# Kernel tuning notes

Hardware: AMD Instinct MI355X
Metric: run time of the kernel (lower is better)

Reference implementation:

```python
import jax, jax.numpy as jnp
import numpy as np

HQ, HKV, HD = 32, 8, 64
ROPE_BASE = 10000.0


def _rope_cos_sin(L):
    # torchtune-style interleaved RoPE cache
    theta = 1.0 / (ROPE_BASE ** (jnp.arange(0, HD, 2, dtype=jnp.float32) / HD))  # [HD/2]
    ang = jnp.arange(L, dtype=jnp.float32)[:, None] * theta[None, :]             # [L, HD/2]
    return jnp.cos(ang)[None, :, None, :], jnp.sin(ang)[None, :, None, :]        # [1,L,1,HD/2]


def _apply_rope(t, cos, sin):
    # t: [B, L, H, HD]; pairs are interleaved along last dim
    x = t.reshape(t.shape[:-1] + (HD // 2, 2))
    x0, x1 = x[..., 0], x[..., 1]
    out = jnp.stack([x0 * cos - x1 * sin, x1 * cos + x0 * sin], axis=-1)
    return out.reshape(t.shape)


def setup_inputs() -> dict:
    key = jax.random.key(0)
    k1, k2, k3 = jax.random.split(key, 3)
    B, L, D = 2, 2048, 2048
    x = jax.random.normal(k1, (B, L, D), dtype=jnp.float32)
    w_qkv = jax.random.normal(k2, ((HQ + 2 * HKV) * HD, D), dtype=jnp.float32) * 0.02
    w_o = jax.random.normal(k3, (D, D), dtype=jnp.float32) * 0.02
    return {"x": x, "w_qkv": w_qkv, "w_o": w_o}


def reference(x, w_qkv, w_o):
    B, L, D = x.shape
    G = HQ // HKV  # q heads per kv head
    qkv = x @ w_qkv.T  # [B, L, (HQ+2*HKV)*HD]
    q = qkv[..., : HQ * HD].reshape(B, L, HQ, HD)
    k = qkv[..., HQ * HD : (HQ + HKV) * HD].reshape(B, L, HKV, HD)
    v = qkv[..., (HQ + HKV) * HD :].reshape(B, L, HKV, HD)

    cos, sin = _rope_cos_sin(L)
    q = _apply_rope(q, cos, sin)
    k = _apply_rope(k, cos, sin)

    # GQA: q head h attends with kv head h // G
    q = q.transpose(0, 2, 1, 3).reshape(B, HKV, G, L, HD)
    k = k.transpose(0, 2, 1, 3)  # [B, HKV, L, HD]
    v = v.transpose(0, 2, 1, 3)

    scale = 1.0 / jnp.sqrt(jnp.float32(HD))
    scores = jnp.einsum('bhgqd,bhkd->bhgqk', q, k) * scale  # [B,HKV,G,L,L]
    causal = jnp.tril(jnp.ones((L, L), dtype=bool))
    scores = jnp.where(causal, scores, jnp.finfo(scores.dtype).min)
    attn = jax.nn.softmax(scores, axis=-1)
    y = jnp.einsum('bhgqk,bhkd->bhgqd', attn, v)            # [B,HKV,G,L,HD]
    y = y.reshape(B, HQ, L, HD).transpose(0, 2, 1, 3).reshape(B, L, D)
    return y @ w_o.T
```

## Files before the change

### kernel.cpp

```cpp
#include <hip/hip_runtime.h>

typedef __attribute__((ext_vector_type(8))) short bf16x8;
typedef __attribute__((ext_vector_type(4))) float f32x4;

__device__ __forceinline__ float bf2f(unsigned short u) {
  unsigned int x = ((unsigned int)u) << 16;
  float f; __builtin_memcpy(&f, &x, 4); return f;
}
__device__ __forceinline__ unsigned short f2bf(float f) {
  unsigned int x; __builtin_memcpy(&x, &f, 4);
  unsigned int lsb = (x >> 16) & 1u;
  x += 0x7fffu + lsb;
  return (unsigned short)(x >> 16);
}
__device__ __forceinline__ unsigned short f2bf_trunc(float f) {
  unsigned int x; __builtin_memcpy(&x, &f, 4);
  return (unsigned short)(x >> 16);
}
__device__ __forceinline__ float exp2_raw(float x) {
  float r;
  asm("v_exp_f32 %0, %1" : "=v"(r) : "v"(x));
  return r;
}
__device__ __forceinline__ void gload16(const unsigned short* g, unsigned short* l) {
  __builtin_amdgcn_global_load_lds(
      (const __attribute__((address_space(1))) unsigned int*)g,
      (__attribute__((address_space(3))) unsigned int*)l, 16, 0, 0);
}

__global__ __launch_bounds__(256) void cvt_bf16(const float* __restrict__ in,
                                                unsigned short* __restrict__ out, int n8) {
  for (int i = blockIdx.x * blockDim.x + threadIdx.x; i < n8;
       i += (int)(gridDim.x * blockDim.x)) {
    const float4* p = (const float4*)(in + (size_t)i * 8);
    float4 a = p[0], b = p[1];
    union { bf16x8 v; unsigned short u[8]; } o;
    o.u[0] = f2bf(a.x); o.u[1] = f2bf(a.y); o.u[2] = f2bf(a.z); o.u[3] = f2bf(a.w);
    o.u[4] = f2bf(b.x); o.u[5] = f2bf(b.y); o.u[6] = f2bf(b.z); o.u[7] = f2bf(b.w);
    *(bf16x8*)(out + (size_t)i * 8) = o.v;
  }
}

template <int F32OUT>
__global__ __launch_bounds__(256) void gemm_bt(const unsigned short* __restrict__ A,
                                               const unsigned short* __restrict__ B,
                                               void* __restrict__ Cp, int N) {
  __shared__ unsigned short sA[128 * 32];
  __shared__ unsigned short sB[128 * 32];
  const int t = threadIdx.x;
  const int lane = t & 63, w = t >> 6;
  const int wm = w >> 1, wn = w & 1;
  const int l16 = lane & 15, hi = lane >> 4;
  const int m0 = blockIdx.y * 128, n0 = blockIdx.x * 128;

  f32x4 zero = {0.f, 0.f, 0.f, 0.f};
  f32x4 acc[4][4];
#pragma unroll
  for (int mi = 0; mi < 4; ++mi)
#pragma unroll
    for (int ni = 0; ni < 4; ++ni) acc[mi][ni] = zero;

  const int srow = t >> 2;
  const int scol = (t & 3) * 8;
  const unsigned short* gA0 = A + (size_t)(m0 + srow) * 2048 + scol;
  const unsigned short* gB0 = B + (size_t)(n0 + srow) * 2048 + scol;

  int offA[4], offB[4];
#pragma unroll
  for (int i = 0; i < 4; ++i) {
    offA[i] = (wm * 64 + i * 16 + l16) * 32 + hi * 8;
    offB[i] = (wn * 64 + i * 16 + l16) * 32 + hi * 8;
  }

  for (int k0 = 0; k0 < 2048; k0 += 32) {
    __syncthreads();
    gload16(gA0 + k0, &sA[t * 8]);
    gload16(gA0 + (size_t)64 * 2048 + k0, &sA[2048 + t * 8]);
    gload16(gB0 + k0, &sB[t * 8]);
    gload16(gB0 + (size_t)64 * 2048 + k0, &sB[2048 + t * 8]);
    __syncthreads();
    bf16x8 af[4], bfr[4];
#pragma unroll
    for (int i = 0; i < 4; ++i) af[i] = *(const bf16x8*)&sA[offA[i]];
#pragma unroll
    for (int i = 0; i < 4; ++i) bfr[i] = *(const bf16x8*)&sB[offB[i]];
#pragma unroll
    for (int mi = 0; mi < 4; ++mi)
#pragma unroll
      for (int ni = 0; ni < 4; ++ni)
        acc[mi][ni] = __builtin_amdgcn_mfma_f32_16x16x32_bf16(af[mi], bfr[ni], acc[mi][ni], 0, 0, 0);
  }

  const int rowb = m0 + wm * 64 + hi * 4;
  const int colb = n0 + wn * 64 + l16;
#pragma unroll
  for (int mi = 0; mi < 4; ++mi)
#pragma unroll
    for (int ni = 0; ni < 4; ++ni)
#pragma unroll
      for (int r = 0; r < 4; ++r) {
        size_t idx = (size_t)(rowb + mi * 16 + r) * N + colb + ni * 16;
        if (F32OUT) ((float*)Cp)[idx] = acc[mi][ni][r];
        else        ((unsigned short*)Cp)[idx] = f2bf(acc[mi][ni][r]);
      }
}

__global__ __launch_bounds__(256) void rope_qk(const unsigned short* __restrict__ qkv,
                                               unsigned short* __restrict__ q,
                                               unsigned short* __restrict__ k) {
  int tid = blockIdx.x * 256 + threadIdx.x;
  int l = tid & 2047;
  int rest = tid >> 11;
  int b = rest & 1;
  int h = rest >> 1;
  const unsigned short* src = qkv + (size_t)(b * 2048 + l) * 3072 + h * 64;
  union { uint4 v[8]; unsigned short u[64]; } buf;
#pragma unroll
  for (int i = 0; i < 8; ++i) buf.v[i] = ((const uint4*)src)[i];
  const float sc = (h < 32) ? 0.125f * 1.44269504088896f : 1.0f;
#pragma unroll
  for (int j = 0; j < 32; ++j) {
    float fr = exp2f(-(float)j * 0.41524101186092033f);
    float ang = (float)l * fr;
    float sn, cs;
    sincosf(ang, &sn, &cs);
    float x0 = bf2f(buf.u[2 * j]), x1 = bf2f(buf.u[2 * j + 1]);
    float y0 = (x0 * cs - x1 * sn) * sc;
    float y1 = (x1 * cs + x0 * sn) * sc;
    buf.u[2 * j] = f2bf(y0);
    buf.u[2 * j + 1] = f2bf(y1);
  }
  unsigned short* dst = (h < 32) ? (q + ((size_t)(b * 32 + h) * 2048 + l) * 64)
                                 : (k + ((size_t)(b * 8 + h - 32) * 2048 + l) * 64);
#pragma unroll
  for (int i = 0; i < 8; ++i) ((uint4*)dst)[i] = buf.v[i];
}

__global__ __launch_bounds__(256) void vtrans(const unsigned short* __restrict__ qkv,
                                              unsigned short* __restrict__ vt) {
  __shared__ unsigned short sT[64 * 72];
  const int t = threadIdx.x;
  const int bh = blockIdx.y;
  const int b = bh >> 3, h = bh & 7;
  const int l0 = blockIdx.x * 64;
  const int c = t & 7, i0 = t >> 3;
#pragma unroll
  for (int pp = 0; pp < 2; ++pp) {
    int i = i0 + pp * 32;
    const unsigned short* src =
        qkv + (size_t)(b * 2048 + l0 + i) * 3072 + 2560 + h * 64 + c * 8;
    union { bf16x8 v; unsigned short u[8]; } x;
    x.v = *(const bf16x8*)src;
#pragma unroll
    for (int e = 0; e < 8; ++e) sT[(c * 8 + e) * 72 + i] = x.u[e];
  }
  __syncthreads();
  const int d = t >> 2, ic = (t & 3) * 16;
  unsigned short* dst = vt + ((size_t)(b * 8 + h) * 64 + d) * 2048 + l0 + ic;
  *(bf16x8*)dst = *(const bf16x8*)&sT[d * 72 + ic];
  *(bf16x8*)(dst + 8) = *(const bf16x8*)&sT[d * 72 + ic + 8];
}

__global__ __launch_bounds__(256) void attn(const unsigned short* __restrict__ Q,
                                            const unsigned short* __restrict__ K,
                                            const unsigned short* __restrict__ VT,
                                            unsigned short* __restrict__ Y) {
  __shared__ unsigned short sK[128 * 64];
  __shared__ unsigned short sV[64 * 128];
  __shared__ unsigned short sP[4][32 * 136];
  const int t = threadIdx.x, lane = t & 63, w = t >> 6;
  const int l16 = lane & 15, hi = lane >> 4;
  const int pi = blockIdx.y;
  const int head = blockIdx.x;
  const int b = head >> 5, hq = head & 31, hkv = hq >> 2;
  const unsigned short* kp = K + (size_t)(b * 8 + hkv) * 2048 * 64;
  const unsigned short* vp = VT + (size_t)(b * 8 + hkv) * 64 * 2048;
  unsigned short* sPw = sP[w];
  f32x4 zero = {0.f, 0.f, 0.f, 0.f};

#pragma unroll
  for (int phase = 0; phase < 2; ++phase) {
    const int qb = phase ? (15 - pi) : pi;
    const int q0 = qb * 128 + w * 32;
    const unsigned short* qp = Q + ((size_t)(b * 32 + hq) * 2048 + q0) * 64;

    bf16x8 qf[2][2];
#pragma unroll
    for (int mi = 0; mi < 2; ++mi)
#pragma unroll
      for (int ks = 0; ks < 2; ++ks)
        qf[mi][ks] = *(const bf16x8*)(qp + (size_t)(mi * 16 + l16) * 64 + ks * 32 + hi * 8);

    f32x4 o[2][4];
    float lsum[2][4];
#pragma unroll
    for (int mi = 0; mi < 2; ++mi) {
#pragma unroll
      for (int ni = 0; ni < 4; ++ni) o[mi][ni] = zero;
#pragma unroll
      for (int r = 0; r < 4; ++r) lsum[mi][r] = 0.f;
    }

    const int nt = qb + 1;
    for (int tt = 0; tt < nt; ++tt) {
      const int c0 = tt * 128;
      __syncthreads();
#pragma unroll
      for (int i = 0; i < 4; ++i) {
        int c = i * 256 + t;
        int row = c >> 3, cb = c & 7;
        gload16(kp + (size_t)(c0 + row) * 64 + ((cb ^ (row & 7)) * 8), &sK[c * 8]);
      }
#pragma unroll
      for (int i = 0; i < 4; ++i) {
        int c = i * 256 + t;
        int d = c >> 4, cb = c & 15;
        gload16(vp + (size_t)d * 2048 + c0 + ((cb ^ (d & 15)) * 8), &sV[c * 8]);
      }
      __syncthreads();

#pragma unroll
      for (int h = 0; h < 2; ++h) {
        const int c0h = c0 + h * 64;
        if (c0h > q0) break;
        f32x4 sc[2][4];
#pragma unroll
        for (int mi = 0; mi < 2; ++mi)
#pragma unroll
          for (int ni = 0; ni < 4; ++ni) sc[mi][ni] = zero;
#pragma unroll
        for (int ni = 0; ni < 4; ++ni) {
          const int krow = h * 64 + ni * 16 + l16;
          bf16x8 k0f = *(const bf16x8*)&sK[krow * 64 + ((hi ^ (l16 & 7)) * 8)];
          bf16x8 k1f = *(const bf16x8*)&sK[krow * 64 + (((4 + hi) ^ (l16 & 7)) * 8)];
#pragma unroll
          for (int mi = 0; mi < 2; ++mi) {
            sc[mi][ni] = __builtin_amdgcn_mfma_f32_16x16x32_bf16(qf[mi][0], k0f, sc[mi][ni], 0, 0, 0);
            sc[mi][ni] = __builtin_amdgcn_mfma_f32_16x16x32_bf16(qf[mi][1], k1f, sc[mi][ni], 0, 0, 0);
          }
        }
        if (c0h + 64 > q0) {
#pragma unroll
          for (int mi = 0; mi < 2; ++mi)
#pragma unroll
            for (int ni = 0; ni < 4; ++ni)
#pragma unroll
              for (int r = 0; r < 4; ++r) {
                int col = c0h + ni * 16 + l16;
                int row = q0 + mi * 16 + hi * 4 + r;
                if (col > row) sc[mi][ni][r] = -1e30f;
              }
        }
#pragma unroll
        for (int mi = 0; mi < 2; ++mi)
#pragma unroll
          for (int ni = 0; ni < 4; ++ni)
#pragma unroll
            for (int r = 0; r < 4; ++r) {
              float p = exp2_raw(sc[mi][ni][r]);
              lsum[mi][r] += p;
              sPw[(mi * 16 + hi * 4 + r) * 136 + h * 64 + ni * 16 + l16] = f2bf_trunc(p);
            }
      }
#pragma unroll
      for (int ks = 0; ks < 4; ++ks) {
        if (c0 + ks * 32 > q0) break;
        bf16x8 pa[2];
#pragma unroll
        for (int mi = 0; mi < 2; ++mi)
          pa[mi] = *(const bf16x8*)&sPw[(mi * 16 + l16) * 136 + ks * 32 + hi * 8];
#pragma unroll
        for (int ni = 0; ni < 4; ++ni) {
          const int d = ni * 16 + l16;
          bf16x8 vb = *(const bf16x8*)&sV[d * 128 + (((ks * 4 + hi) ^ l16) * 8)];
#pragma unroll
          for (int mi = 0; mi < 2; ++mi)
            o[mi][ni] = __builtin_amdgcn_mfma_f32_16x16x32_bf16(pa[mi], vb, o[mi][ni], 0, 0, 0);
        }
      }
    }
#pragma unroll
    for (int mi = 0; mi < 2; ++mi) {
#pragma unroll
      for (int msk = 1; msk <= 8; msk <<= 1)
#pragma unroll
        for (int r = 0; r < 4; ++r) lsum[mi][r] += __shfl_xor(lsum[mi][r], msk);
      float inv[4];
#pragma unroll
      for (int r = 0; r < 4; ++r) inv[r] = 1.f / lsum[mi][r];
#pragma unroll
      for (int ni = 0; ni < 4; ++ni)
#pragma unroll
        for (int r = 0; r < 4; ++r) {
          int row = q0 + mi * 16 + hi * 4 + r;
          Y[(size_t)(b * 2048 + row) * 2048 + hq * 64 + ni * 16 + l16] =
              f2bf(o[mi][ni][r] * inv[r]);
        }
    }
  }
}

extern "C" void kernel_launch(void* const* d_in, const int* in_sizes, int n_in,
                              void* d_out, int out_size, void* d_ws, size_t ws_size,
                              hipStream_t stream) {
  const float* x    = (const float*)d_in[0];
  const float* wqkv = (const float*)d_in[1];
  const float* wo   = (const float*)d_in[2];
  float* out = (float*)d_out;

  char* ws = (char*)d_ws;
  unsigned short* xb   = (unsigned short*)(ws);
  unsigned short* wqb  = (unsigned short*)(ws + 16777216);
  unsigned short* wob  = (unsigned short*)(ws + 29360128);
  unsigned short* qkvb = (unsigned short*)(ws + 37748736);
  unsigned short* qb   = (unsigned short*)(ws + 62914560);
  unsigned short* kb   = (unsigned short*)(ws + 79691776);
  unsigned short* vtb  = (unsigned short*)(ws + 83886080);
  unsigned short* yb = xb;

  cvt_bf16<<<2048, 256, 0, stream>>>(x, xb, 8388608 / 8);
  cvt_bf16<<<2048, 256, 0, stream>>>(wqkv, wqb, 6291456 / 8);
  gemm_bt<0><<<dim3(3072 / 128, 4096 / 128), 256, 0, stream>>>(xb, wqb, qkvb, 3072);
  cvt_bf16<<<2048, 256, 0, stream>>>(wo, wob, 4194304 / 8);
  rope_qk<<<640, 256, 0, stream>>>(qkvb, qb, kb);
  vtrans<<<dim3(32, 16), 256, 0, stream>>>(qkvb, vtb);
  attn<<<dim3(64, 8), 256, 0, stream>>>(qb, kb, vtb, yb);
  gemm_bt<1><<<dim3(2048 / 128, 4096 / 128), 256, 0, stream>>>(yb, wob, out, 2048);
}
```

Baseline: 212.1 us.

## Share K/V tile loads across paired query blocks and fuse conversion kernels

The attention kernel now processes both paired causal query blocks (pi and 15-pi) in a single pass over key/value tiles, so every K/V tile is loaded into shared memory once and reused by both blocks instead of being reloaded in a second phase. This removes about half of the K/V global-to-LDS traffic and barriers for the early tiles, but it doubles the live accumulator and Q-fragment registers, which may reduce occupancy. Separately, the three fp32-to-bf16 conversion launches are merged into one kernel to cut launch overhead.

```diff
diff --git a/kernel.cpp b/kernel.cpp
--- a/kernel.cpp
+++ b/kernel.cpp
@@ -28,16 +28,25 @@
       (__attribute__((address_space(3))) unsigned int*)l, 16, 0, 0);
 }
 
-__global__ __launch_bounds__(256) void cvt_bf16(const float* __restrict__ in,
-                                                unsigned short* __restrict__ out, int n8) {
-  for (int i = blockIdx.x * blockDim.x + threadIdx.x; i < n8;
-       i += (int)(gridDim.x * blockDim.x)) {
-    const float4* p = (const float4*)(in + (size_t)i * 8);
+__global__ __launch_bounds__(256) void cvt3(const float* __restrict__ x,
+                                            const float* __restrict__ wq,
+                                            const float* __restrict__ wo,
+                                            unsigned short* __restrict__ xb,
+                                            unsigned short* __restrict__ wqb,
+                                            unsigned short* __restrict__ wob) {
+  const int N0 = 1048576, N1 = 786432, N2 = 524288;
+  for (int i = blockIdx.x * 256 + threadIdx.x; i < N0 + N1 + N2;
+       i += (int)(gridDim.x * 256)) {
+    const float* in; unsigned short* out; int j;
+    if (i < N0)            { in = x;  out = xb;  j = i; }
+    else if (i < N0 + N1)  { in = wq; out = wqb; j = i - N0; }
+    else                   { in = wo; out = wob; j = i - N0 - N1; }
+    const float4* p = (const float4*)(in + (size_t)j * 8);
     float4 a = p[0], b = p[1];
     union { bf16x8 v; unsigned short u[8]; } o;
     o.u[0] = f2bf(a.x); o.u[1] = f2bf(a.y); o.u[2] = f2bf(a.z); o.u[3] = f2bf(a.w);
     o.u[4] = f2bf(b.x); o.u[5] = f2bf(b.y); o.u[6] = f2bf(b.z); o.u[7] = f2bf(b.w);
-    *(bf16x8*)(out + (size_t)i * 8) = o.v;
+    *(bf16x8*)(out + (size_t)j * 8) = o.v;
   }
 }
 
@@ -159,6 +168,74 @@
   unsigned short* dst = vt + ((size_t)(b * 8 + h) * 64 + d) * 2048 + l0 + ic;
   *(bf16x8*)dst = *(const bf16x8*)&sT[d * 72 + ic];
   *(bf16x8*)(dst + 8) = *(const bf16x8*)&sT[d * 72 + ic + 8];
+}
+
+__device__ __forceinline__ void attn_step(const unsigned short* __restrict__ sK,
+                                          const unsigned short* __restrict__ sV,
+                                          unsigned short* __restrict__ sPw,
+                                          const bf16x8 (&qf)[2][2],
+                                          f32x4 (&o)[2][4], float (&lsum)[2][4],
+                                          int q0, int c0, int l16, int hi) {
+  f32x4 zero = {0.f, 0.f, 0.f, 0.f};
+#pragma unroll
+  for (int h = 0; h < 2; ++h) {
+    const int c0h = c0 + h * 64;
+    if (c0h > q0) break;
+    f32x4 sc[2][4];
+#pragma unroll
+    for (int mi = 0; mi < 2; ++mi)
+#pragma unroll
+      for (int ni = 0; ni < 4; ++ni) sc[mi][ni] = zero;
+#pragma unroll
+    for (int ni = 0; ni < 4; ++ni) {
+      const int krow = h * 64 + ni * 16 + l16;
+      bf16x8 k0f = *(const bf16x8*)&sK[krow * 64 + ((hi ^ (l16 & 7)) * 8)];
+      bf16x8 k1f = *(const bf16x8*)&sK[krow * 64 + (((4 + hi) ^ (l16 & 7)) * 8)];
+#pragma unroll
+      for (int mi = 0; mi < 2; ++mi) {
+        sc[mi][ni] = __builtin_amdgcn_mfma_f32_16x16x32_bf16(qf[mi][0], k0f, sc[mi][ni], 0, 0, 0);
+        sc[mi][ni] = __builtin_amdgcn_mfma_f32_16x16x32_bf16(qf[mi][1], k1f, sc[mi][ni], 0, 0, 0);
+      }
+    }
+    if (c0h + 64 > q0) {
+#pragma unroll
+      for (int mi = 0; mi < 2; ++mi)
+#pragma unroll
+        for (int ni = 0; ni < 4; ++ni)
+#pragma unroll
+          for (int r = 0; r < 4; ++r) {
+            int col = c0h + ni * 16 + l16;
+            int row = q0 + mi * 16 + hi * 4 + r;
+            if (col > row) sc[mi][ni][r] = -1e30f;
+          }
+    }
+#pragma unroll
+    for (int mi = 0; mi < 2; ++mi)
+#pragma unroll
+      for (int ni = 0; ni < 4; ++ni)
+#pragma unroll
+        for (int r = 0; r < 4; ++r) {
+          float p = exp2_raw(sc[mi][ni][r]);
+          lsum[mi][r] += p;
+          sPw[(mi * 16 + hi * 4 + r) * 136 + h * 64 + ni * 16 + l16] = f2bf_trunc(p);
+        }
+  }
+#pragma unroll
+  for (int ks = 0; ks < 4; ++ks) {
+    if (c0 + ks * 32 > q0) break;
+    bf16x8 pa[2];
+#pragma unroll
+    for (int mi = 0; mi < 2; ++mi)
+      pa[mi] = *(const bf16x8*)&sPw[(mi * 16 + l16) * 136 + ks * 32 + hi * 8];
+#pragma unroll
+    for (int ni = 0; ni < 4; ++ni) {
+      const int d = ni * 16 + l16;
+      bf16x8 vb = *(const bf16x8*)&sV[d * 128 + (((ks * 4 + hi) ^ l16) * 8)];
+#pragma unroll
+      for (int mi = 0; mi < 2; ++mi)
+        o[mi][ni] = __builtin_amdgcn_mfma_f32_16x16x32_bf16(pa[mi], vb, o[mi][ni], 0, 0, 0);
+    }
+  }
 }
 
 __global__ __launch_bounds__(256) void attn(const unsigned short* __restrict__ Q,
@@ -178,116 +255,67 @@
   unsigned short* sPw = sP[w];
   f32x4 zero = {0.f, 0.f, 0.f, 0.f};
 
-#pragma unroll
-  for (int phase = 0; phase < 2; ++phase) {
-    const int qb = phase ? (15 - pi) : pi;
-    const int q0 = qb * 128 + w * 32;
-    const unsigned short* qp = Q + ((size_t)(b * 32 + hq) * 2048 + q0) * 64;
-
-    bf16x8 qf[2][2];
-#pragma unroll
-    for (int mi = 0; mi < 2; ++mi)
-#pragma unroll
-      for (int ks = 0; ks < 2; ++ks)
-        qf[mi][ks] = *(const bf16x8*)(qp + (size_t)(mi * 16 + l16) * 64 + ks * 32 + hi * 8);
-
-    f32x4 o[2][4];
-    float lsum[2][4];
+  const int q0A = pi * 128 + w * 32;
+  const int q0B = (15 - pi) * 128 + w * 32;
+  const unsigned short* qpA = Q + ((size_t)(b * 32 + hq) * 2048 + q0A) * 64;
+  const unsigned short* qpB = Q + ((size_t)(b * 32 + hq) * 2048 + q0B) * 64;
+
+  bf16x8 qfA[2][2], qfB[2][2];
+#pragma unroll
+  for (int mi = 0; mi < 2; ++mi)
+#pragma unroll
+    for (int ks = 0; ks < 2; ++ks) {
+      qfA[mi][ks] = *(const bf16x8*)(qpA + (size_t)(mi * 16 + l16) * 64 + ks * 32 + hi * 8);
+      qfB[mi][ks] = *(const bf16x8*)(qpB + (size_t)(mi * 16 + l16) * 64 + ks * 32 + hi * 8);
+    }
+
+  f32x4 oA[2][4], oB[2][4];
+  float lsA[2][4], lsB[2][4];
+#pragma unroll
+  for (int mi = 0; mi < 2; ++mi) {
+#pragma unroll
+    for (int ni = 0; ni < 4; ++ni) { oA[mi][ni] = zero; oB[mi][ni] = zero; }
+#pragma unroll
+    for (int r = 0; r < 4; ++r) { lsA[mi][r] = 0.f; lsB[mi][r] = 0.f; }
+  }
+
+  const int ntt = 16 - pi;
+  for (int tt = 0; tt < ntt; ++tt) {
+    const int c0 = tt * 128;
+    __syncthreads();
+#pragma unroll
+    for (int i = 0; i < 4; ++i) {
+      int c = i * 256 + t;
+      int row = c >> 3, cb = c & 7;
+      gload16(kp + (size_t)(c0 + row) * 64 + ((cb ^ (row & 7)) * 8), &sK[c * 8]);
+    }
+#pragma unroll
+    for (int i = 0; i < 4; ++i) {
+      int c = i * 256 + t;
+      int d = c >> 4, cb = c & 15;
+      gload16(vp + (size_t)d * 2048 + c0 + ((cb ^ (d & 15)) * 8), &sV[c * 8]);
+    }
+    __syncthreads();
+
+    if (tt <= pi)
+      attn_step(sK, sV, sPw, qfA, oA, lsA, q0A, c0, l16, hi);
+    attn_step(sK, sV, sPw, qfB, oB, lsB, q0B, c0, l16, hi);
+  }
+
+#pragma unroll
+  for (int e = 0; e < 2; ++e) {
+    f32x4 (&o)[2][4] = e ? oB : oA;
+    float (&ls)[2][4] = e ? lsB : lsA;
+    const int q0 = e ? q0B : q0A;
 #pragma unroll
     for (int mi = 0; mi < 2; ++mi) {
 #pragma unroll
-      for (int ni = 0; ni < 4; ++ni) o[mi][ni] = zero;
-#pragma unroll
-      for (int r = 0; r < 4; ++r) lsum[mi][r] = 0.f;
-    }
-
-    const int nt = qb + 1;
-    for (int tt = 0; tt < nt; ++tt) {
-      const int c0 = tt * 128;
-      __syncthreads();
-#pragma unroll
-      for (int i = 0; i < 4; ++i) {
-        int c = i * 256 + t;
-        int row = c >> 3, cb = c & 7;
-        gload16(kp + (size_t)(c0 + row) * 64 + ((cb ^ (row & 7)) * 8), &sK[c * 8]);
-      }
-#pragma unroll
-      for (int i = 0; i < 4; ++i) {
-        int c = i * 256 + t;
-        int d = c >> 4, cb = c & 15;
-        gload16(vp + (size_t)d * 2048 + c0 + ((cb ^ (d & 15)) * 8), &sV[c * 8]);
-      }
-      __syncthreads();
-
-#pragma unroll
-      for (int h = 0; h < 2; ++h) {
-        const int c0h = c0 + h * 64;
-        if (c0h > q0) break;
-        f32x4 sc[2][4];
-#pragma unroll
-        for (int mi = 0; mi < 2; ++mi)
-#pragma unroll
-          for (int ni = 0; ni < 4; ++ni) sc[mi][ni] = zero;
-#pragma unroll
-        for (int ni = 0; ni < 4; ++ni) {
-          const int krow = h * 64 + ni * 16 + l16;
-          bf16x8 k0f = *(const bf16x8*)&sK[krow * 64 + ((hi ^ (l16 & 7)) * 8)];
-          bf16x8 k1f = *(const bf16x8*)&sK[krow * 64 + (((4 + hi) ^ (l16 & 7)) * 8)];
-#pragma unroll
-          for (int mi = 0; mi < 2; ++mi) {
-            sc[mi][ni] = __builtin_amdgcn_mfma_f32_16x16x32_bf16(qf[mi][0], k0f, sc[mi][ni], 0, 0, 0);
-            sc[mi][ni] = __builtin_amdgcn_mfma_f32_16x16x32_bf16(qf[mi][1], k1f, sc[mi][ni], 0, 0, 0);
-          }
-        }
-        if (c0h + 64 > q0) {
-#pragma unroll
-          for (int mi = 0; mi < 2; ++mi)
-#pragma unroll
-            for (int ni = 0; ni < 4; ++ni)
-#pragma unroll
-              for (int r = 0; r < 4; ++r) {
-                int col = c0h + ni * 16 + l16;
-                int row = q0 + mi * 16 + hi * 4 + r;
-                if (col > row) sc[mi][ni][r] = -1e30f;
-              }
-        }
-#pragma unroll
-        for (int mi = 0; mi < 2; ++mi)
-#pragma unroll
-          for (int ni = 0; ni < 4; ++ni)
-#pragma unroll
-            for (int r = 0; r < 4; ++r) {
-              float p = exp2_raw(sc[mi][ni][r]);
-              lsum[mi][r] += p;
-              sPw[(mi * 16 + hi * 4 + r) * 136 + h * 64 + ni * 16 + l16] = f2bf_trunc(p);
-            }
-      }
-#pragma unroll
-      for (int ks = 0; ks < 4; ++ks) {
-        if (c0 + ks * 32 > q0) break;
-        bf16x8 pa[2];
-#pragma unroll
-        for (int mi = 0; mi < 2; ++mi)
-          pa[mi] = *(const bf16x8*)&sPw[(mi * 16 + l16) * 136 + ks * 32 + hi * 8];
-#pragma unroll
-        for (int ni = 0; ni < 4; ++ni) {
-          const int d = ni * 16 + l16;
-          bf16x8 vb = *(const bf16x8*)&sV[d * 128 + (((ks * 4 + hi) ^ l16) * 8)];
-#pragma unroll
-          for (int mi = 0; mi < 2; ++mi)
-            o[mi][ni] = __builtin_amdgcn_mfma_f32_16x16x32_bf16(pa[mi], vb, o[mi][ni], 0, 0, 0);
-        }
-      }
-    }
-#pragma unroll
-    for (int mi = 0; mi < 2; ++mi) {
-#pragma unroll
       for (int msk = 1; msk <= 8; msk <<= 1)
 #pragma unroll
-        for (int r = 0; r < 4; ++r) lsum[mi][r] += __shfl_xor(lsum[mi][r], msk);
+        for (int r = 0; r < 4; ++r) ls[mi][r] += __shfl_xor(ls[mi][r], msk);
       float inv[4];
 #pragma unroll
-      for (int r = 0; r < 4; ++r) inv[r] = 1.f / lsum[mi][r];
+      for (int r = 0; r < 4; ++r) inv[r] = 1.f / ls[mi][r];
 #pragma unroll
       for (int ni = 0; ni < 4; ++ni)
 #pragma unroll
@@ -318,10 +346,8 @@
   unsigned short* vtb  = (unsigned short*)(ws + 83886080);
   unsigned short* yb = xb;
 
-  cvt_bf16<<<2048, 256, 0, stream>>>(x, xb, 8388608 / 8);
-  cvt_bf16<<<2048, 256, 0, stream>>>(wqkv, wqb, 6291456 / 8);
+  cvt3<<<2048, 256, 0, stream>>>(x, wqkv, wo, xb, wqb, wob);
   gemm_bt<0><<<dim3(3072 / 128, 4096 / 128), 256, 0, stream>>>(xb, wqb, qkvb, 3072);
-  cvt_bf16<<<2048, 256, 0, stream>>>(wo, wob, 4194304 / 8);
   rope_qk<<<640, 256, 0, stream>>>(qkvb, qb, kb);
   vtrans<<<dim3(32, 16), 256, 0, stream>>>(qkvb, vtb);
   attn<<<dim3(64, 8), 256, 0, stream>>>(qb, kb, vtb, yb);
```

Result: slower. 233.8 us (+10.2%).
